# Kernel tuning notes

Measured on AMD Instinct MI355X. Metric: run time of the kernel, lower is better.

The kernel has to match this reference:

```python
import jax, jax.numpy as jnp
import numpy as np

N, E = 50000, 800000
IN, HID, H, OUT = 128, 32, 8, 64
HD = HID * H  # 256
EPS = 1e-5


def _p(key, shape, scale=0.05):
    return jax.random.normal(key, shape, dtype=jnp.float32) * scale


def setup_inputs() -> dict:
    key = jax.random.key(0)
    ks = jax.random.split(key, 32)
    inp = {
        'x': jax.random.normal(ks[0], (N, IN), dtype=jnp.float32),
        'edge_index': jax.random.randint(ks[1], (2, E), 0, N, dtype=jnp.int64),
        'edge_attr': jax.random.normal(ks[2], (E, 1), dtype=jnp.float32),
        # layer 1 (TransformerConv: in=128 -> heads*hid=256)
        'Wq1': _p(ks[3], (IN, HD)), 'bq1': jnp.zeros((HD,), jnp.float32),
        'Wk1': _p(ks[4], (IN, HD)), 'bk1': jnp.zeros((HD,), jnp.float32),
        'Wv1': _p(ks[5], (IN, HD)), 'bv1': jnp.zeros((HD,), jnp.float32),
        'We1': _p(ks[6], (1, HD)),  # lin_edge, no bias in PyG
        'Ws1': _p(ks[7], (IN, HD)), 'bs1': jnp.zeros((HD,), jnp.float32),  # root/skip
        'lnw1': jnp.ones((HD,), jnp.float32), 'lnb1': jnp.zeros((HD,), jnp.float32),
        # layer 2 (in=256 -> 256)
        'Wq2': _p(ks[8], (HD, HD)), 'bq2': jnp.zeros((HD,), jnp.float32),
        'Wk2': _p(ks[9], (HD, HD)), 'bk2': jnp.zeros((HD,), jnp.float32),
        'Wv2': _p(ks[10], (HD, HD)), 'bv2': jnp.zeros((HD,), jnp.float32),
        'We2': _p(ks[11], (1, HD)),
        'Ws2': _p(ks[12], (HD, HD)), 'bs2': jnp.zeros((HD,), jnp.float32),
        'lnw2': jnp.ones((HD,), jnp.float32), 'lnb2': jnp.zeros((HD,), jnp.float32),
        # output linear 256 -> 64
        'Wo': _p(ks[13], (HD, OUT)), 'bo': jnp.zeros((OUT,), jnp.float32),
    }
    return inp


def transformer_conv(x, src, dst, edge_attr, Wq, bq, Wk, bk, Wv, bv, We, Ws, bs):
    n = x.shape[0]
    q = (x @ Wq + bq).reshape(n, H, HID)
    k = (x @ Wk + bk).reshape(n, H, HID)
    v = (x @ Wv + bv).reshape(n, H, HID)
    e = (edge_attr @ We).reshape(-1, H, HID)            # [E,H,d]
    kj = k[src] + e                                     # gather + edge key
    score = jnp.einsum('ehd,ehd->eh', q[dst], kj) / np.sqrt(HID)  # [E,H]
    # segment softmax over destination nodes
    m = jax.ops.segment_max(score, dst, num_segments=n)  # [N,H]
    ex = jnp.exp(score - m[dst])
    s = jax.ops.segment_sum(ex, dst, num_segments=n)
    alpha = ex / s[dst]                                  # [E,H]
    msg = alpha[..., None] * (v[src] + e)                # [E,H,d]
    out = jax.ops.segment_sum(msg, dst, num_segments=n).reshape(n, HD)
    return out + x @ Ws + bs                             # root weight skip


def graph_layernorm(x, w, b):
    # PyG LayerNorm, mode='graph': global mean/std over all nodes & features
    xc = x - x.mean()
    out = xc / (xc.std() + EPS)
    return out * w + b


def reference(x, edge_index, edge_attr,
              Wq1, bq1, Wk1, bk1, Wv1, bv1, We1, Ws1, bs1, lnw1, lnb1,
              Wq2, bq2, Wk2, bk2, Wv2, bv2, We2, Ws2, bs2, lnw2, lnb2,
              Wo, bo):
    src, dst = edge_index[0], edge_index[1]
    h = transformer_conv(x, src, dst, edge_attr, Wq1, bq1, Wk1, bk1, Wv1, bv1, We1, Ws1, bs1)
    h = jax.nn.elu(graph_layernorm(h, lnw1, lnb1))
    h = transformer_conv(h, src, dst, edge_attr, Wq2, bq2, Wk2, bk2, Wv2, bv2, We2, Ws2, bs2)
    h = jax.nn.elu(graph_layernorm(h, lnw2, lnb2))
    return h @ Wo + bo
```

## Files before the change

kernel.cpp:

```cpp
#include <hip/hip_runtime.h>
#include <hip/hip_fp16.h>
#include <math.h>

#define IN_DIM 128
#define HD 256
#define EPSLN 1e-5f

typedef _Float16 half8 __attribute__((ext_vector_type(8)));
typedef float f32x4 __attribute__((ext_vector_type(4)));
typedef float f32x2 __attribute__((ext_vector_type(2)));

__device__ inline void store4(float* p, float4 o) { *(float4*)p = o; }
__device__ inline void store4(__half* p, float4 o) {
    union { uint2 u; __half2 h[2]; } s;
    s.h[0] = __floats2half2_rn(o.x, o.y);
    s.h[1] = __floats2half2_rn(o.z, o.w);
    *(uint2*)p = s.u;
}
__device__ inline float4 h4_to_f4(uint2 u) {
    union { unsigned int w; __half2 h; } a, b;
    a.w = u.x; b.w = u.y;
    float2 lo = __half22float2(a.h), hi = __half22float2(b.h);
    return make_float4(lo.x, lo.y, hi.x, hi.y);
}
__device__ inline unsigned int f4_to_fp8x4(float a, float b, float c, float d) {
    int v = 0;
    v = __builtin_amdgcn_cvt_pk_fp8_f32(a, b, v, false);
    v = __builtin_amdgcn_cvt_pk_fp8_f32(c, d, v, true);
    return (unsigned int)v;
}
__device__ inline float4 fp8x4_to_f4(unsigned int u) {
    f32x2 lo = __builtin_amdgcn_cvt_pk_f32_fp8((int)u, false);
    f32x2 hi = __builtin_amdgcn_cvt_pk_f32_fp8((int)u, true);
    return make_float4(lo.x, lo.y, hi.x, hi.y);
}

__device__ inline void async_copy16(const __half* g, _Float16* l) {
    __builtin_amdgcn_global_load_lds(
        (const __attribute__((address_space(1))) void*)g,
        (__attribute__((address_space(3))) void*)l,
        16, 0, 0);
}

__device__ inline void unpermute_col(int n, int& sel, int& c) {
    if (n < 256) { sel = 0; c = n; }
    else if (n < 768) {
        int j = n - 256, chunk = j >> 3, w = j & 7;
        if (w < 4) { sel = 1; c = chunk * 4 + w; }
        else       { sel = 2; c = chunk * 4 + w - 4; }
    } else { sel = 3; c = n - 768; }
}

__global__ void prep_k(
    const float4* __restrict__ x, __half* __restrict__ xh, int total4,
    const int* __restrict__ dst, int* __restrict__ counts, int* __restrict__ rank, int E,
    const float* __restrict__ Wq1, const float* __restrict__ Wk1,
    const float* __restrict__ Wv1, const float* __restrict__ Ws1,
    const float* __restrict__ Wq2, const float* __restrict__ Wk2,
    const float* __restrict__ Wv2, const float* __restrict__ Ws2,
    const float* __restrict__ Wo,
    const float* __restrict__ bq1, const float* __restrict__ bk1,
    const float* __restrict__ bv1, const float* __restrict__ bs1,
    const float* __restrict__ bq2, const float* __restrict__ bk2,
    const float* __restrict__ bv2, const float* __restrict__ bs2,
    __half* __restrict__ Wc1, __half* __restrict__ Wc2, __half* __restrict__ Wot,
    float* __restrict__ bc1, float* __restrict__ bc2)
{
    int idx = blockIdx.x * 256 + threadIdx.x;
    if (idx < total4) store4(xh + (size_t)idx * 4, x[idx]);
    if (idx < E) rank[idx] = atomicAdd(&counts[dst[idx]], 1);
    if (idx < 131072) {
        int n = idx >> 7, k = idx & 127;
        int sel, c; unpermute_col(n, sel, c);
        const float* W = (sel == 0) ? Wq1 : (sel == 1) ? Wk1 : (sel == 2) ? Wv1 : Ws1;
        Wc1[idx] = __float2half(W[(size_t)k * 256 + c]);
    } else if (idx < 393216) {
        int j = idx - 131072;
        int n = j >> 8, k = j & 255;
        int sel, c; unpermute_col(n, sel, c);
        const float* W = (sel == 0) ? Wq2 : (sel == 1) ? Wk2 : (sel == 2) ? Wv2 : Ws2;
        Wc2[j] = __float2half(W[(size_t)k * 256 + c]);
    } else if (idx < 409600) {
        int j = idx - 393216;
        int n = j >> 8, k = j & 255;
        Wot[j] = __float2half(Wo[(size_t)k * 64 + n]);
    } else if (idx < 410624) {
        int n = idx - 409600;
        int sel, c; unpermute_col(n, sel, c);
        const float* b = (sel == 0) ? bq1 : (sel == 1) ? bk1 : (sel == 2) ? bv1 : bs1;
        bc1[n] = b[c];
    } else if (idx < 411648) {
        int n = idx - 410624;
        int sel, c; unpermute_col(n, sel, c);
        const float* b = (sel == 0) ? bq2 : (sel == 1) ? bk2 : (sel == 2) ? bv2 : bs2;
        bc2[n] = b[c];
    }
}

#define BM 128
#define BN 128
#define BK 64
#define TROWB 272

__global__ __launch_bounds__(256) void gemm_mfma(
    const __half* __restrict__ A, const __half* __restrict__ Wt,
    const float* __restrict__ bias, __half* __restrict__ C,
    unsigned char* __restrict__ kv8,
    int M, int K, int Nc)
{
    __shared__ char smem[BM * TROWB];
    _Float16* As = (_Float16*)smem;
    _Float16* Bs = (_Float16*)(smem + 16384);

    int tid = threadIdx.x;
    int lane = tid & 63, w = tid >> 6;
    int wm = w >> 1, wn = w & 1;
    int quad = lane >> 4, l16 = lane & 15;
    int row0 = blockIdx.x * BM, col0 = blockIdx.y * BN;

    f32x4 acc[4][4];
#pragma unroll
    for (int i = 0; i < 4; i++)
#pragma unroll
        for (int j = 0; j < 4; j++) acc[i][j] = (f32x4){0.f, 0.f, 0.f, 0.f};

    int srow = lane >> 3;
    int schunk = lane & 7;

    for (int k0 = 0; k0 < K; k0 += BK) {
#pragma unroll
        for (int t = 0; t < 4; t++) {
            int r = w * 32 + t * 8 + srow;
            int gr = row0 + r; if (gr > M - 1) gr = M - 1;
            int gchunk = schunk ^ (r & 7);
            async_copy16(&A[(size_t)gr * K + k0 + gchunk * 8], &As[(w * 32 + t * 8) * 64]);
        }
#pragma unroll
        for (int t = 0; t < 4; t++) {
            int r = w * 32 + t * 8 + srow;
            int gc = col0 + r; if (gc > Nc - 1) gc = Nc - 1;
            int gchunk = schunk ^ (r & 7);
            async_copy16(&Wt[(size_t)gc * K + k0 + gchunk * 8], &Bs[(w * 32 + t * 8) * 64]);
        }
        __syncthreads();

#pragma unroll
        for (int ks = 0; ks < 2; ks++) {
            half8 af[4], bf[4];
#pragma unroll
            for (int i = 0; i < 4; i++) {
                int ra = wm * 64 + i * 16 + l16;
                af[i] = *(half8*)&As[ra * 64 + (((ks * 4 + quad) ^ (ra & 7)) * 8)];
                int rb = wn * 64 + i * 16 + l16;
                bf[i] = *(half8*)&Bs[rb * 64 + (((ks * 4 + quad) ^ (rb & 7)) * 8)];
            }
#pragma unroll
            for (int i = 0; i < 4; i++)
#pragma unroll
                for (int j = 0; j < 4; j++)
                    acc[i][j] = __builtin_amdgcn_mfma_f32_16x16x32_f16(af[i], bf[j], acc[i][j], 0, 0, 0);
        }
        __syncthreads();
    }

#pragma unroll
    for (int j = 0; j < 4; j++) {
        int tcol = wn * 64 + j * 16 + l16;
        float bb = (col0 + tcol < Nc) ? bias[col0 + tcol] : 0.f;
#pragma unroll
        for (int i = 0; i < 4; i++) {
#pragma unroll
            for (int r = 0; r < 4; r++) {
                int trow = wm * 64 + i * 16 + quad * 4 + r;
                ((__half*)(smem + trow * TROWB))[tcol] = __float2half(acc[i][j][r] + bb);
            }
        }
    }
    __syncthreads();
    bool iskv = (col0 >= 256) && (col0 < 768);
    int crow = tid >> 4, cchunk = tid & 15;
    for (int p = 0; p < 8; p++) {
        int trow = p * 16 + crow;
        int grow = row0 + trow;
        if (grow >= M) continue;
        uint4 val = *(uint4*)(smem + trow * TROWB + cchunk * 16);
        if (iskv) {
            float4 lo = h4_to_f4(make_uint2(val.x, val.y));
            float4 hi = h4_to_f4(make_uint2(val.z, val.w));
            uint2 o8;
            o8.x = f4_to_fp8x4(lo.x, lo.y, lo.z, lo.w);
            o8.y = f4_to_fp8x4(hi.x, hi.y, hi.z, hi.w);
            *(uint2*)&kv8[(size_t)grow * 512 + (col0 - 256) + cchunk * 8] = o8;
        } else {
            *(uint4*)&C[(size_t)grow * Nc + col0 + cchunk * 8] = val;
        }
    }
}

__global__ __launch_bounds__(256) void gemm_out_k(
    const __half* __restrict__ A, const __half* __restrict__ Wot,
    const float* __restrict__ bias, float* __restrict__ D, int M)
{
    __shared__ _Float16 As[128 * 64];
    __shared__ _Float16 Bs[64 * 64];
    int tid = threadIdx.x;
    int lane = tid & 63, w = tid >> 6;
    int quad = lane >> 4, l16 = lane & 15;
    int row0 = blockIdx.x * 128;
    const int K = 256;

    f32x4 acc[2][4];
#pragma unroll
    for (int i = 0; i < 2; i++)
#pragma unroll
        for (int j = 0; j < 4; j++) acc[i][j] = (f32x4){0.f, 0.f, 0.f, 0.f};

    int srow = lane >> 3;
    int schunk = lane & 7;

    for (int k0 = 0; k0 < K; k0 += BK) {
#pragma unroll
        for (int t = 0; t < 4; t++) {
            int r = w * 32 + t * 8 + srow;
            int gr = row0 + r; if (gr > M - 1) gr = M - 1;
            int gchunk = schunk ^ (r & 7);
            async_copy16(&A[(size_t)gr * K + k0 + gchunk * 8], &As[(w * 32 + t * 8) * 64]);
        }
#pragma unroll
        for (int t = 0; t < 2; t++) {
            int r = w * 16 + t * 8 + srow;
            int gchunk = schunk ^ (r & 7);
            async_copy16(&Wot[(size_t)r * K + k0 + gchunk * 8], &Bs[(w * 16 + t * 8) * 64]);
        }
        __syncthreads();

#pragma unroll
        for (int ks = 0; ks < 2; ks++) {
            half8 af[2], bf[4];
#pragma unroll
            for (int i = 0; i < 2; i++) {
                int ra = w * 32 + i * 16 + l16;
                af[i] = *(half8*)&As[ra * 64 + (((ks * 4 + quad) ^ (ra & 7)) * 8)];
            }
#pragma unroll
            for (int j = 0; j < 4; j++) {
                int rb = j * 16 + l16;
                bf[j] = *(half8*)&Bs[rb * 64 + (((ks * 4 + quad) ^ (rb & 7)) * 8)];
            }
#pragma unroll
            for (int i = 0; i < 2; i++)
#pragma unroll
                for (int j = 0; j < 4; j++)
                    acc[i][j] = __builtin_amdgcn_mfma_f32_16x16x32_f16(af[i], bf[j], acc[i][j], 0, 0, 0);
        }
        __syncthreads();
    }

#pragma unroll
    for (int i = 0; i < 2; i++) {
#pragma unroll
        for (int j = 0; j < 4; j++) {
            int gcol = j * 16 + l16;
            float bb = bias[gcol];
#pragma unroll
            for (int r = 0; r < 4; r++) {
                int grow = row0 + w * 32 + i * 16 + quad * 4 + r;
                if (grow < M) D[(size_t)grow * 64 + gcol] = acc[i][j][r] + bb;
            }
        }
    }
}

__global__ __launch_bounds__(1024) void scan_k(const int* __restrict__ counts,
                                               int* __restrict__ offs, int n)
{
    __shared__ int wsum[16];
    __shared__ int wpre[16];
    int tid = threadIdx.x, lane = tid & 63, wid = tid >> 6;
    int per = (n + 1023) / 1024;
    int start = tid * per, end = min(start + per, n);
    int sum = 0;
    for (int i = start; i < end; i++) sum += counts[i];
    int v = sum;
#pragma unroll
    for (int d = 1; d < 64; d <<= 1) {
        int t = __shfl_up(v, (unsigned)d, 64);
        if (lane >= d) v += t;
    }
    if (lane == 63) wsum[wid] = v;
    __syncthreads();
    if (tid == 0) {
        int acc = 0;
        for (int i = 0; i < 16; i++) { wpre[i] = acc; acc += wsum[i]; }
    }
    __syncthreads();
    int pre = wpre[wid] + v - sum;
    for (int i = start; i < end; i++) { offs[i] = pre; pre += counts[i]; }
    if (end == n && start <= n) offs[n] = pre;
}

__global__ void scatter_k(const int* __restrict__ src, const int* __restrict__ dst,
                          const float* __restrict__ attr, const int* __restrict__ offs,
                          const int* __restrict__ rank, int2* __restrict__ edat, int E)
{
    int e = blockIdx.x * 256 + threadIdx.x;
    if (e < E) {
        int p = offs[dst[e]] + rank[e];
        edat[p] = make_int2(src[e], __float_as_int(attr[e]));
    }
}

__global__ __launch_bounds__(256) void attn_k(
    const uint2* __restrict__ q2, const uint2* __restrict__ kv8u2,
    const float* __restrict__ We,
    __half* __restrict__ hwork, const int2* __restrict__ edat,
    const int* __restrict__ offs,
    double* __restrict__ stats, int n, int nGroups)
{
    int lane = threadIdx.x & 63;
    int wid = threadIdx.x >> 6;
    float4 we = ((const float4*)We)[lane];
    float tsum = 0.f, tsq = 0.f;

    for (int g = blockIdx.x; g < nGroups; g += gridDim.x) {
        int node = g * 4 + wid;
        if (node >= n) continue;
        float4 qv = h4_to_f4(q2[(size_t)node * 256 + lane]);
        float qwe = qv.x * we.x + qv.y * we.y + qv.z * we.z + qv.w * we.w;
        qwe += __shfl_xor(qwe, 1);
        qwe += __shfl_xor(qwe, 2);
        qwe += __shfl_xor(qwe, 4);

        float4 accv = make_float4(0.f, 0.f, 0.f, 0.f);
        float sat = 0.f;
        float m = -INFINITY, l = 0.f;
        int i0 = offs[node], i1 = offs[node + 1];

        for (int i = i0; i < i1; i += 8) {
            int cnt = i1 - i;
            float atv[8];
            int   si[8];
#pragma unroll
            for (int u = 0; u < 8; u++) {
                int2 ed = edat[(u < cnt) ? (i + u) : i];
                si[u] = ed.x;
                atv[u] = __int_as_float(ed.y);
            }
            uint2 kvv[8];
#pragma unroll
            for (int u = 0; u < 8; u++)
                kvv[u] = kv8u2[(size_t)si[u] * 64 + lane];

            float pv[8];
#pragma unroll
            for (int u = 0; u < 8; u++) {
                float4 kv = fp8x4_to_f4(kvv[u].x);
                float p = qv.x * kv.x + qv.y * kv.y + qv.z * kv.z + qv.w * kv.w;
                p += __shfl_xor(p, 1);
                p += __shfl_xor(p, 2);
                p += __shfl_xor(p, 4);
                p = fmaf(atv[u], qwe, p) * 0.17677669529663687f;
                pv[u] = (u < cnt) ? p : -INFINITY;
            }

            float m01 = fmaxf(pv[0], pv[1]), m23 = fmaxf(pv[2], pv[3]);
            float m45 = fmaxf(pv[4], pv[5]), m67 = fmaxf(pv[6], pv[7]);
            float pmax = fmaxf(fmaxf(m01, m23), fmaxf(m45, m67));
            float mn = fmaxf(m, pmax);
            float corr = __expf(m - mn);
            l *= corr;
            sat *= corr;
            accv.x *= corr; accv.y *= corr; accv.z *= corr; accv.w *= corr;
#pragma unroll
            for (int u = 0; u < 8; u++) {
                float wgt = __expf(pv[u] - mn);
                l += wgt;
                sat = fmaf(wgt, atv[u], sat);
                float4 vv = fp8x4_to_f4(kvv[u].y);
                accv.x = fmaf(wgt, vv.x, accv.x);
                accv.y = fmaf(wgt, vv.y, accv.y);
                accv.z = fmaf(wgt, vv.z, accv.z);
                accv.w = fmaf(wgt, vv.w, accv.w);
            }
            m = mn;
        }

        float inv = (l > 0.f) ? 1.f / l : 0.f;
        float4 sk = h4_to_f4(q2[(size_t)node * 256 + 192 + lane]);
        float sw = sat * inv;
        float4 o;
        o.x = fmaf(accv.x, inv, fmaf(sw, we.x, sk.x));
        o.y = fmaf(accv.y, inv, fmaf(sw, we.y, sk.y));
        o.z = fmaf(accv.z, inv, fmaf(sw, we.z, sk.z));
        o.w = fmaf(accv.w, inv, fmaf(sw, we.w, sk.w));
        store4(hwork + (size_t)node * 256 + lane * 4, o);
        tsum += o.x + o.y + o.z + o.w;
        tsq += o.x * o.x + o.y * o.y + o.z * o.z + o.w * o.w;
    }

#pragma unroll
    for (int d = 1; d < 64; d <<= 1) {
        tsum += __shfl_xor(tsum, d);
        tsq += __shfl_xor(tsq, d);
    }
    __shared__ float red[8];
    if (lane == 0) { red[wid] = tsum; red[4 + wid] = tsq; }
    __syncthreads();
    if (threadIdx.x == 0) {
        double s = (double)red[0] + (double)red[1] + (double)red[2] + (double)red[3];
        double sq = (double)red[4] + (double)red[5] + (double)red[6] + (double)red[7];
        atomicAdd(&stats[0], s);
        atomicAdd(&stats[1], sq);
    }
}

__global__ __launch_bounds__(256) void ln_apply(
    const uint2* __restrict__ in, __half* __restrict__ out,
    const float4* __restrict__ w4, const float4* __restrict__ b4,
    const double* __restrict__ stats, double cnt, int total4)
{
    int base = (blockIdx.x * 256 + threadIdx.x) * 4;
    if (base >= total4) return;
    double mu = stats[0] / cnt;
    double var = stats[1] / cnt - mu * mu;
    if (var < 0.0) var = 0.0;
    float mean = (float)mu;
    float inv = (float)(1.0 / (sqrt(var) + (double)EPSLN));
#pragma unroll
    for (int u = 0; u < 4; u++) {
        int i = base + u;
        if (i >= total4) return;
        int c = i & 63;
        float4 xv = h4_to_f4(in[i]);
        float4 w = w4[c], b = b4[c];
        float4 o;
        o.x = fmaf((xv.x - mean) * inv, w.x, b.x);
        o.y = fmaf((xv.y - mean) * inv, w.y, b.y);
        o.z = fmaf((xv.z - mean) * inv, w.z, b.z);
        o.w = fmaf((xv.w - mean) * inv, w.w, b.w);
        o.x = o.x > 0.f ? o.x : expm1f(o.x);
        o.y = o.y > 0.f ? o.y : expm1f(o.y);
        o.z = o.z > 0.f ? o.z : expm1f(o.z);
        o.w = o.w > 0.f ? o.w : expm1f(o.w);
        store4(out + (size_t)i * 4, o);
    }
}

extern "C" void kernel_launch(void* const* d_in, const int* in_sizes, int n_in,
                              void* d_out, int out_size, void* d_ws, size_t ws_size,
                              hipStream_t stream)
{
    const float* x      = (const float*)d_in[0];
    const int*   ei     = (const int*)d_in[1];
    const float* eattr  = (const float*)d_in[2];
    const float* Wq1 = (const float*)d_in[3];  const float* bq1 = (const float*)d_in[4];
    const float* Wk1 = (const float*)d_in[5];  const float* bk1 = (const float*)d_in[6];
    const float* Wv1 = (const float*)d_in[7];  const float* bv1 = (const float*)d_in[8];
    const float* We1 = (const float*)d_in[9];
    const float* Ws1 = (const float*)d_in[10]; const float* bs1 = (const float*)d_in[11];
    const float* lnw1 = (const float*)d_in[12]; const float* lnb1 = (const float*)d_in[13];
    const float* Wq2 = (const float*)d_in[14]; const float* bq2 = (const float*)d_in[15];
    const float* Wk2 = (const float*)d_in[16]; const float* bk2 = (const float*)d_in[17];
    const float* Wv2 = (const float*)d_in[18]; const float* bv2 = (const float*)d_in[19];
    const float* We2 = (const float*)d_in[20];
    const float* Ws2 = (const float*)d_in[21]; const float* bs2 = (const float*)d_in[22];
    const float* lnw2 = (const float*)d_in[23]; const float* lnb2 = (const float*)d_in[24];
    const float* Wo  = (const float*)d_in[25]; const float* bo  = (const float*)d_in[26];

    const int N = in_sizes[0] / IN_DIM;
    const int E = in_sizes[2];
    const int* esrc = ei;
    const int* edst = ei + E;

    char* ws = (char*)d_ws;
    size_t off = 0;
    auto alloc = [&](size_t bytes) -> char* {
        char* p = ws + off;
        off += (bytes + 255) / 256 * 256;
        return p;
    };
    int*    counts = (int*)alloc((size_t)N * 4);
    double* stats  = (double*)alloc(64);
    size_t zbytes = off;
    int*    rank   = (int*)alloc((size_t)E * 4);
    int*    offs   = (int*)alloc((size_t)(N + 1) * 4);
    int2*   edat   = (int2*)alloc((size_t)E * 8);
    __half* xh     = (__half*)alloc((size_t)N * IN_DIM * 2);
    __half* qkvs   = (__half*)alloc((size_t)N * 1024 * 2);
    unsigned char* kv8 = (unsigned char*)alloc((size_t)N * 512);
    __half* hwork  = (__half*)alloc((size_t)N * HD * 2);
    __half* hio    = (__half*)alloc((size_t)N * HD * 2);
    __half* Wc1    = (__half*)alloc((size_t)1024 * IN_DIM * 2);
    __half* Wc2    = (__half*)alloc((size_t)1024 * HD * 2);
    __half* Wot    = (__half*)alloc((size_t)64 * HD * 2);
    float*  bc1    = (float*)alloc(1024 * 4);
    float*  bc2    = (float*)alloc(1024 * 4);

    hipMemsetAsync(d_ws, 0, zbytes, stream);

    int total4x = N * (IN_DIM / 4);
    int prepWork = total4x > E ? total4x : E;
    if (prepWork < 411648) prepWork = 411648;
    prep_k<<<(prepWork + 255) / 256, 256, 0, stream>>>(
        (const float4*)x, xh, total4x, edst, counts, rank, E,
        Wq1, Wk1, Wv1, Ws1, Wq2, Wk2, Wv2, Ws2, Wo,
        bq1, bk1, bv1, bs1, bq2, bk2, bv2, bs2,
        Wc1, Wc2, Wot, bc1, bc2);

    scan_k<<<1, 1024, 0, stream>>>(counts, offs, N);
    scatter_k<<<(E + 255) / 256, 256, 0, stream>>>(esrc, edst, eattr, offs, rank,
                                                   edat, E);

    dim3 gqkvs((N + BM - 1) / BM, 1024 / BN);
    int nGroups = (N + 3) / 4;
    int gaBlocks = nGroups < 2048 ? nGroups : 2048;
    int total4 = N * (HD / 4);
    dim3 gl((total4 / 4 + 255) / 256);
    dim3 gout((N + 127) / 128);

    gemm_mfma<<<gqkvs, 256, 0, stream>>>(xh, Wc1, bc1, qkvs, kv8, N, IN_DIM, 1024);
    attn_k<<<gaBlocks, 256, 0, stream>>>((const uint2*)qkvs, (const uint2*)kv8, We1,
                                         hwork, edat, offs, stats, N, nGroups);
    ln_apply<<<gl, 256, 0, stream>>>((const uint2*)hwork, hio,
                                     (const float4*)lnw1, (const float4*)lnb1,
                                     stats, (double)N * HD, total4);

    gemm_mfma<<<gqkvs, 256, 0, stream>>>(hio, Wc2, bc2, qkvs, kv8, N, HD, 1024);
    attn_k<<<gaBlocks, 256, 0, stream>>>((const uint2*)qkvs, (const uint2*)kv8, We2,
                                         hwork, edat, offs, stats + 2, N, nGroups);
    ln_apply<<<gl, 256, 0, stream>>>((const uint2*)hwork, hio,
                                     (const float4*)lnw2, (const float4*)lnb2,
                                     stats + 2, (double)N * HD, total4);

    gemm_out_k<<<gout, 256, 0, stream>>>(hio, Wot, bo, (float*)d_out, N);
}
```

Baseline: 621.1 us.

## Double-buffer edge gathers in attention and swizzle GEMM block mapping across XCDs

The attention kernel now prefetches the next batch of 8 edges (edge data plus fp8 K/V rows) while computing the current batch, using two register buffers. Edge indices and attributes are made wave-uniform with readfirstlane. The edge array is padded with 8 zero entries so unconditional over-reads stay in bounds. The QKV GEMM switches to a 1D grid with a remapped block index, so blocks that share rows land on the same XCD for L2 reuse; the cost is higher register pressure in the attention loop.

```diff
diff --git a/kernel.cpp b/kernel.cpp
--- a/kernel.cpp
+++ b/kernel.cpp
@@ -116,7 +116,10 @@
     int lane = tid & 63, w = tid >> 6;
     int wm = w >> 1, wn = w & 1;
     int quad = lane >> 4, l16 = lane & 15;
-    int row0 = blockIdx.x * BM, col0 = blockIdx.y * BN;
+    int nbx = (int)gridDim.x >> 3;
+    int wkr = ((int)blockIdx.x & 7) * nbx + ((int)blockIdx.x >> 3);
+    int row0 = (wkr >> 3) * BM;
+    int col0 = (wkr & 7) * BN;
 
     f32x4 acc[4][4];
 #pragma unroll
@@ -304,6 +307,7 @@
                           const int* __restrict__ rank, int2* __restrict__ edat, int E)
 {
     int e = blockIdx.x * 256 + threadIdx.x;
+    if (e < 8) edat[E + e] = make_int2(0, 0);
     if (e < E) {
         int p = offs[dst[e]] + rank[e];
         edat[p] = make_int2(src[e], __float_as_int(attr[e]));
@@ -334,35 +338,36 @@
         float4 accv = make_float4(0.f, 0.f, 0.f, 0.f);
         float sat = 0.f;
         float m = -INFINITY, l = 0.f;
-        int i0 = offs[node], i1 = offs[node + 1];
-
-        for (int i = i0; i < i1; i += 8) {
-            int cnt = i1 - i;
-            float atv[8];
-            int   si[8];
+        int i0 = __builtin_amdgcn_readfirstlane(offs[node]);
+        int i1 = __builtin_amdgcn_readfirstlane(offs[node + 1]);
+
+        int abA[8], srA[8], abB[8], srB[8];
+        uint2 kvA[8], kvB[8];
+
+        auto LOADB = [&](int base, int* ab_, int* sr_, uint2* kv_) {
 #pragma unroll
             for (int u = 0; u < 8; u++) {
-                int2 ed = edat[(u < cnt) ? (i + u) : i];
-                si[u] = ed.x;
-                atv[u] = __int_as_float(ed.y);
-            }
-            uint2 kvv[8];
+                int2 ed = edat[base + u];
+                sr_[u] = __builtin_amdgcn_readfirstlane(ed.x);
+                ab_[u] = __builtin_amdgcn_readfirstlane(ed.y);
+            }
 #pragma unroll
             for (int u = 0; u < 8; u++)
-                kvv[u] = kv8u2[(size_t)si[u] * 64 + lane];
-
+                kv_[u] = (kv8u2 + (size_t)(unsigned)sr_[u] * 64)[lane];
+        };
+
+        auto COMPUTE = [&](const int* ab_, const uint2* kv_, int cnt) {
             float pv[8];
 #pragma unroll
             for (int u = 0; u < 8; u++) {
-                float4 kv = fp8x4_to_f4(kvv[u].x);
-                float p = qv.x * kv.x + qv.y * kv.y + qv.z * kv.z + qv.w * kv.w;
+                float4 kvf = fp8x4_to_f4(kv_[u].x);
+                float p = qv.x * kvf.x + qv.y * kvf.y + qv.z * kvf.z + qv.w * kvf.w;
                 p += __shfl_xor(p, 1);
                 p += __shfl_xor(p, 2);
                 p += __shfl_xor(p, 4);
-                p = fmaf(atv[u], qwe, p) * 0.17677669529663687f;
+                p = fmaf(__int_as_float(ab_[u]), qwe, p) * 0.17677669529663687f;
                 pv[u] = (u < cnt) ? p : -INFINITY;
             }
-
             float m01 = fmaxf(pv[0], pv[1]), m23 = fmaxf(pv[2], pv[3]);
             float m45 = fmaxf(pv[4], pv[5]), m67 = fmaxf(pv[6], pv[7]);
             float pmax = fmaxf(fmaxf(m01, m23), fmaxf(m45, m67));
@@ -375,14 +380,29 @@
             for (int u = 0; u < 8; u++) {
                 float wgt = __expf(pv[u] - mn);
                 l += wgt;
-                sat = fmaf(wgt, atv[u], sat);
-                float4 vv = fp8x4_to_f4(kvv[u].y);
+                sat = fmaf(wgt, __int_as_float(ab_[u]), sat);
+                float4 vv = fp8x4_to_f4(kv_[u].y);
                 accv.x = fmaf(wgt, vv.x, accv.x);
                 accv.y = fmaf(wgt, vv.y, accv.y);
                 accv.z = fmaf(wgt, vv.z, accv.z);
                 accv.w = fmaf(wgt, vv.w, accv.w);
             }
             m = mn;
+        };
+
+        if (i0 < i1) {
+            int i = i0;
+            LOADB(i, abA, srA, kvA);
+            while (true) {
+                if (i + 8 >= i1) { COMPUTE(abA, kvA, i1 - i); break; }
+                LOADB(i + 8, abB, srB, kvB);
+                COMPUTE(abA, kvA, 8);
+                i += 8;
+                if (i + 8 >= i1) { COMPUTE(abB, kvB, i1 - i); break; }
+                LOADB(i + 8, abA, srA, kvA);
+                COMPUTE(abB, kvB, 8);
+                i += 8;
+            }
         }
 
         float inv = (l > 0.f) ? 1.f / l : 0.f;
@@ -484,7 +504,7 @@
     size_t zbytes = off;
     int*    rank   = (int*)alloc((size_t)E * 4);
     int*    offs   = (int*)alloc((size_t)(N + 1) * 4);
-    int2*   edat   = (int2*)alloc((size_t)E * 8);
+    int2*   edat   = (int2*)alloc((size_t)(E + 8) * 8);
     __half* xh     = (__half*)alloc((size_t)N * IN_DIM * 2);
     __half* qkvs   = (__half*)alloc((size_t)N * 1024 * 2);
     unsigned char* kv8 = (unsigned char*)alloc((size_t)N * 512);
@@ -511,7 +531,8 @@
     scatter_k<<<(E + 255) / 256, 256, 0, stream>>>(esrc, edst, eattr, offs, rank,
                                                    edat, E);
 
-    dim3 gqkvs((N + BM - 1) / BM, 1024 / BN);
+    int nbx = (N + BM - 1) / BM;
+    dim3 gqkvs(nbx * 8);
     int nGroups = (N + 3) / 4;
     int gaBlocks = nGroups < 2048 ? nGroups : 2048;
     int total4 = N * (HD / 4);
```

Result: faster. 572.9 us, median of 2 (-7.8%).
